# Optimization experiments

Hardware: AMD Instinct MI355X
Metric: run time of the kernel (lower is better)

Reference implementation:

```python
import jax, jax.numpy as jnp
import numpy as np

NEG = -9e15

def setup_inputs() -> dict:
    key = jax.random.key(0)
    kH, kA, kW, ka = jax.random.split(key, 4)
    B, N, Din, Dout, Hh = 4, 2048, 128, 32, 8
    H = jax.random.normal(kH, (B, N, Din), dtype=jnp.float32)
    adj = jax.random.randint(kA, (B, N, N), 0, 2, dtype=jnp.int32)
    W = jax.random.normal(kW, (Hh, Din, Dout), dtype=jnp.float32) * (1.0 / np.sqrt(Din))
    a = jax.random.normal(ka, (Hh, 2 * Dout, 1), dtype=jnp.float32) * 0.1
    return {"H": H, "adj": adj, "W": W, "a": a}

def reference(H, adj, W, a):
    # H: [B,N,Din], adj: [B,N,N], W: [h,Din,D], a: [h,2D,1]
    B, N, _ = H.shape
    h, _, D = W.shape
    Wh = jnp.einsum('bni,hio->bhno', H, W)            # [B,h,N,D]
    a1 = a[:, :D, 0]                                   # [h,D] (source/query half)
    a2 = a[:, D:, 0]                                   # [h,D] (neighbor half)
    ei = jnp.einsum('bhnd,hd->bhn', Wh, a1)            # [B,h,N]
    ej = jnp.einsum('bhnd,hd->bhn', Wh, a2)            # [B,h,N]
    e = ei[:, :, :, None] + ej[:, :, None, :]          # [B,h,N,N] == a^T[Wh_i;Wh_j]
    mask = adj[:, None, :, :].astype(bool)             # [B,1,N,N]
    e = jnp.where(mask, e, jnp.float32(NEG))
    alpha = jax.nn.softmax(e, axis=-1)                 # [B,h,N,N]; dropout is identity (eval)
    h_prime = jnp.einsum('bhnm,bhmd->bhnd', alpha, Wh) # [B,h,N,D]
    h_prime = jnp.transpose(h_prime, (0, 2, 1, 3)).reshape(B, N, h * D)
    return jax.nn.relu(h_prime), alpha
```

## Files before the change

kernel.cpp:

```cpp
#include <hip/hip_runtime.h>
#include <stdint.h>

#define BB 4
#define NN 2048
#define DIN 128
#define DOUT 32
#define HH 8
#define NW 64

typedef __bf16 bf16x8 __attribute__((ext_vector_type(8)));
typedef float  f32x4  __attribute__((ext_vector_type(4)));

static __device__ __forceinline__ unsigned short f2b(float f) {
    __bf16 h = (__bf16)f;
    return __builtin_bit_cast(unsigned short, h);
}
static __device__ __forceinline__ float b2f(unsigned short u) {
    union { unsigned int i; float f; } v; v.i = ((unsigned int)u) << 16; return v.f;
}

__global__ __launch_bounds__(256) void k_wht(const float* __restrict__ Hg,
                                             const float* __restrict__ Wg,
                                             unsigned short* __restrict__ WhT)
{
    __shared__ float Hs[DIN * 16];
    const int t  = threadIdx.x;
    const int b  = blockIdx.x >> 7;
    const int n0 = (blockIdx.x & 127) << 4;

    {
        const int r = t >> 4, i0 = (t & 15) << 3;
        const float4* hp = (const float4*)(Hg + ((size_t)(b * NN + n0 + r)) * DIN + i0);
        float4 u0 = hp[0], u1 = hp[1];
        float vv[8] = { u0.x, u0.y, u0.z, u0.w, u1.x, u1.y, u1.z, u1.w };
#pragma unroll
        for (int j = 0; j < 8; j++) Hs[(i0 + j) * 16 + r] = vv[j];
    }
    __syncthreads();

    const int h = t >> 5, d = t & 31;
    f32x4 a0 = {0,0,0,0}, a1 = {0,0,0,0}, a2 = {0,0,0,0}, a3 = {0,0,0,0};
    const float* wp = Wg + h * DIN * DOUT + d;
#pragma unroll 8
    for (int i = 0; i < DIN; i++) {
        float wv = wp[i * DOUT];
        const f32x4* hr = (const f32x4*)&Hs[i * 16];
        a0 += wv * hr[0];
        a1 += wv * hr[1];
        a2 += wv * hr[2];
        a3 += wv * hr[3];
    }
    float v[16] = { a0[0],a0[1],a0[2],a0[3], a1[0],a1[1],a1[2],a1[3],
                    a2[0],a2[1],a2[2],a2[3], a3[0],a3[1],a3[2],a3[3] };
    unsigned int pw[8];
#pragma unroll
    for (int j = 0; j < 8; j++)
        pw[j] = (unsigned int)f2b(v[2*j]) | ((unsigned int)f2b(v[2*j+1]) << 16);
    uint4* dst = (uint4*)(WhT + ((size_t)((b * HH + h) * DOUT + d)) * NN + n0);
    dst[0] = make_uint4(pw[0], pw[1], pw[2], pw[3]);
    dst[1] = make_uint4(pw[4], pw[5], pw[6], pw[7]);
}

__global__ __launch_bounds__(256) void k_bits(const int* __restrict__ adj,
                                              unsigned long long* __restrict__ BM)
{
    size_t tg = (size_t)blockIdx.x * 256 + threadIdx.x;
    unsigned long long m = __ballot(adj[tg] != 0);
    if ((threadIdx.x & 63) == 0) BM[tg >> 6] = m;
}

__global__ __launch_bounds__(256) void k_e(const unsigned short* __restrict__ WhT,
                                           const float* __restrict__ ag,
                                           float* __restrict__ E)
{
    const int blk = blockIdx.x;
    const int bh  = blk >> 3;
    const int h   = bh & 7;
    const int m   = ((blk & 7) << 8) + threadIdx.x;
    const unsigned short* wp = WhT + (size_t)(bh * DOUT) * NN + m;
    float acc = 0.f;
#pragma unroll 8
    for (int dd = 0; dd < DOUT; dd++)
        acc += b2f(wp[(size_t)dd * NN]) * ag[h * 2 * DOUT + DOUT + dd];
    E[(size_t)bh * NN + m] = __expf(acc);
}

__global__ __launch_bounds__(256) void k_main(const float* __restrict__ E,
                                              const unsigned int* __restrict__ BM,
                                              const unsigned short* __restrict__ WhT,
                                              float* __restrict__ out0,
                                              float* __restrict__ out1)
{
    __shared__ float        Es[NN];
    __shared__ unsigned int bits[16][68];
    __shared__ float        red[16][17];
    __shared__ float        invS[16];
    __shared__ __align__(16) __bf16 Ast[4][16][72];
    __shared__ __align__(16) __bf16 Bst[4][32][72];
    __shared__ float        Cred[4][16][33];

    const int t   = threadIdx.x;
    const int bh  = blockIdx.x >> 7;
    const int b   = bh >> 3, h = bh & 7;
    const int n0  = (blockIdx.x & 127) << 4;

    {
        const f32x4* src = (const f32x4*)(E + (size_t)bh * NN);
        f32x4* dst = (f32x4*)Es;
        dst[t]       = src[t];
        dst[t + 256] = src[t + 256];
        const int r = t >> 4, w0 = (t & 15) << 2;
        *(uint4*)&bits[r][w0] =
            *(const uint4*)(BM + ((size_t)(b * NN + n0 + r)) * NW + w0);
    }
    __syncthreads();

    {
        const int r = t >> 4, l = t & 15;
        const unsigned int* br = bits[r];
        float s = 0.f;
#pragma unroll 4
        for (int k2 = 0; k2 < NW; k2++) {
            unsigned int wd = br[k2];
            int m = (k2 << 5) + l;
            if ((wd >> l) & 1)        s += Es[m];
            if ((wd >> (l + 16)) & 1) s += Es[m + 16];
        }
        red[r][l] = s;
    }
    __syncthreads();
    if (t < 16) {
        float s = 0.f;
#pragma unroll
        for (int j = 0; j < 16; j++) s += red[t][j];
        invS[t] = 1.0f / s;
    }
    __syncthreads();

    const int w = t >> 6, lane = t & 63;
    const int r2 = lane >> 2, c4 = lane & 3;
    const int quad = lane >> 4, l16 = lane & 15;
    f32x4 acc[2] = { {0,0,0,0}, {0,0,0,0} };
    const size_t out1row = ((size_t)bh * NN + n0 + r2) * NN;
    const unsigned short* wsrc = WhT + ((size_t)bh * DOUT + (lane >> 1)) * NN
                                     + ((lane & 1) << 5);

    for (int c = 0; c < 8; c++) {
        const int m0 = (w << 9) + (c << 6);
        const int mL = m0 + (c4 << 4);

        {
            const float iv = invS[r2];
            const unsigned int wv =
                (bits[r2][(m0 >> 5) + (c4 >> 1)] >> ((c4 & 1) << 4)) & 0xFFFFu;
            const f32x4* ev = (const f32x4*)&Es[mL];
            float* orow = out1 + out1row + mL;
            unsigned int pk[8];
#pragma unroll
            for (int q = 0; q < 4; q++) {
                f32x4 e4 = ev[q];
                f32x4 x;
                x[0] = ((wv >> (4*q + 0)) & 1) ? e4[0] * iv : 0.f;
                x[1] = ((wv >> (4*q + 1)) & 1) ? e4[1] * iv : 0.f;
                x[2] = ((wv >> (4*q + 2)) & 1) ? e4[2] * iv : 0.f;
                x[3] = ((wv >> (4*q + 3)) & 1) ? e4[3] * iv : 0.f;
                *(f32x4*)(orow + (q << 2)) = x;
                pk[2*q]     = (unsigned int)f2b(x[0]) | ((unsigned int)f2b(x[1]) << 16);
                pk[2*q + 1] = (unsigned int)f2b(x[2]) | ((unsigned int)f2b(x[3]) << 16);
            }
            uint4 q0 = make_uint4(pk[0], pk[1], pk[2], pk[3]);
            uint4 q1 = make_uint4(pk[4], pk[5], pk[6], pk[7]);
            *(bf16x8*)&Ast[w][r2][(c4 << 4)]     = __builtin_bit_cast(bf16x8, q0);
            *(bf16x8*)&Ast[w][r2][(c4 << 4) + 8] = __builtin_bit_cast(bf16x8, q1);
        }

        {
            const uint4* s4 = (const uint4*)(wsrc + m0);
            __bf16* dp = &Bst[w][lane >> 1][(lane & 1) << 5];
#pragma unroll
            for (int k = 0; k < 4; k++)
                *(bf16x8*)(dp + 8*k) = __builtin_bit_cast(bf16x8, s4[k]);
        }

#pragma unroll
        for (int ks = 0; ks < 64; ks += 32) {
            bf16x8 af  = *(const bf16x8*)&Ast[w][l16     ][ks + (quad << 3)];
            bf16x8 bf0 = *(const bf16x8*)&Bst[w][l16     ][ks + (quad << 3)];
            bf16x8 bf1 = *(const bf16x8*)&Bst[w][l16 + 16][ks + (quad << 3)];
            acc[0] = __builtin_amdgcn_mfma_f32_16x16x32_bf16(af, bf0, acc[0], 0, 0, 0);
            acc[1] = __builtin_amdgcn_mfma_f32_16x16x32_bf16(af, bf1, acc[1], 0, 0, 0);
        }
    }

#pragma unroll
    for (int hf = 0; hf < 2; hf++)
#pragma unroll
        for (int i = 0; i < 4; i++)
            Cred[w][(quad << 2) + i][l16 + (hf << 4)] = acc[hf][i];
    __syncthreads();
#pragma unroll
    for (int e = t; e < 512; e += 256) {
        const int r = e >> 5, d = e & 31;
        float v = Cred[0][r][d] + Cred[1][r][d] + Cred[2][r][d] + Cred[3][r][d];
        out0[((size_t)(b * NN + n0 + r)) * (HH * DOUT) + h * DOUT + d] = fmaxf(v, 0.f);
    }
}

extern "C" void kernel_launch(void* const* d_in, const int* in_sizes, int n_in,
                              void* d_out, int out_size, void* d_ws, size_t ws_size,
                              hipStream_t stream)
{
    const float* Hg  = (const float*)d_in[0];
    const int*   adj = (const int*)d_in[1];
    const float* Wg  = (const float*)d_in[2];
    const float* ag  = (const float*)d_in[3];

    float* out0 = (float*)d_out;
    float* out1 = out0 + (size_t)BB * NN * HH * DOUT;

    char* ws = (char*)d_ws;
    unsigned short* WhT = (unsigned short*)ws;
    float*          E   = (float*)(ws + (size_t)BB*HH*DOUT*NN*2);
    unsigned int*   BM  = (unsigned int*)(ws + (size_t)BB*HH*DOUT*NN*2
                                             + (size_t)BB*HH*NN*4);

    k_wht <<<BB * (NN/16),         256, 0, stream>>>(Hg, Wg, WhT);
    k_bits<<<(BB * NN * NN) / 256, 256, 0, stream>>>(adj, (unsigned long long*)BM);
    k_e   <<<BB * HH * (NN/256),   256, 0, stream>>>(WhT, ag, E);
    k_main<<<BB * HH * (NN/16),    256, 0, stream>>>(E, BM, WhT, out0, out1);
}
```

Measured before the change: 709.0 us.

## Fuse exp-score kernel into projection and feed MFMA straight from registers

Computes the neighbor attention term and its exponential inside the projection kernel, which removes the separate E kernel and its re-read of WhT. The main kernel now builds MFMA A and B operands directly in registers, using a lane mapping that matches the MFMA input layout, so the shared-memory staging buffers are gone. Alpha rows are written with nontemporal stores. The cost is extra shared memory and a barrier in the projection kernel, plus uncoalesced-looking direct global loads of WhT for the B operand.

```diff
diff --git a/kernel.cpp b/kernel.cpp
--- a/kernel.cpp
+++ b/kernel.cpp
@@ -15,15 +15,15 @@
     __bf16 h = (__bf16)f;
     return __builtin_bit_cast(unsigned short, h);
 }
-static __device__ __forceinline__ float b2f(unsigned short u) {
-    union { unsigned int i; float f; } v; v.i = ((unsigned int)u) << 16; return v.f;
-}
 
 __global__ __launch_bounds__(256) void k_wht(const float* __restrict__ Hg,
                                              const float* __restrict__ Wg,
-                                             unsigned short* __restrict__ WhT)
+                                             const float* __restrict__ ag,
+                                             unsigned short* __restrict__ WhT,
+                                             float* __restrict__ E)
 {
     __shared__ float Hs[DIN * 16];
+    __shared__ float ejred[HH][16][36];
     const int t  = threadIdx.x;
     const int b  = blockIdx.x >> 7;
     const int n0 = (blockIdx.x & 127) << 4;
@@ -59,6 +59,18 @@
     uint4* dst = (uint4*)(WhT + ((size_t)((b * HH + h) * DOUT + d)) * NN + n0);
     dst[0] = make_uint4(pw[0], pw[1], pw[2], pw[3]);
     dst[1] = make_uint4(pw[4], pw[5], pw[6], pw[7]);
+
+    const float a2v = ag[h * 2 * DOUT + DOUT + d];
+#pragma unroll
+    for (int j = 0; j < 16; j++) ejred[h][j][d] = v[j] * a2v;
+    __syncthreads();
+    if (t < 128) {
+        const int hh = t >> 4, j = t & 15;
+        const f32x4* rp = (const f32x4*)&ejred[hh][j][0];
+        f32x4 s4 = rp[0] + rp[1] + rp[2] + rp[3] + rp[4] + rp[5] + rp[6] + rp[7];
+        float s = s4[0] + s4[1] + s4[2] + s4[3];
+        E[((size_t)(b * HH + hh)) * NN + n0 + j] = __expf(s);
+    }
 }
 
 __global__ __launch_bounds__(256) void k_bits(const int* __restrict__ adj,
@@ -67,22 +79,6 @@
     size_t tg = (size_t)blockIdx.x * 256 + threadIdx.x;
     unsigned long long m = __ballot(adj[tg] != 0);
     if ((threadIdx.x & 63) == 0) BM[tg >> 6] = m;
-}
-
-__global__ __launch_bounds__(256) void k_e(const unsigned short* __restrict__ WhT,
-                                           const float* __restrict__ ag,
-                                           float* __restrict__ E)
-{
-    const int blk = blockIdx.x;
-    const int bh  = blk >> 3;
-    const int h   = bh & 7;
-    const int m   = ((blk & 7) << 8) + threadIdx.x;
-    const unsigned short* wp = WhT + (size_t)(bh * DOUT) * NN + m;
-    float acc = 0.f;
-#pragma unroll 8
-    for (int dd = 0; dd < DOUT; dd++)
-        acc += b2f(wp[(size_t)dd * NN]) * ag[h * 2 * DOUT + DOUT + dd];
-    E[(size_t)bh * NN + m] = __expf(acc);
 }
 
 __global__ __launch_bounds__(256) void k_main(const float* __restrict__ E,
@@ -95,8 +91,6 @@
     __shared__ unsigned int bits[16][68];
     __shared__ float        red[16][17];
     __shared__ float        invS[16];
-    __shared__ __align__(16) __bf16 Ast[4][16][72];
-    __shared__ __align__(16) __bf16 Bst[4][32][72];
     __shared__ float        Cred[4][16][33];
 
     const int t   = threadIdx.x;
@@ -138,58 +132,59 @@
     __syncthreads();
 
     const int w = t >> 6, lane = t & 63;
-    const int r2 = lane >> 2, c4 = lane & 3;
     const int quad = lane >> 4, l16 = lane & 15;
     f32x4 acc[2] = { {0,0,0,0}, {0,0,0,0} };
-    const size_t out1row = ((size_t)bh * NN + n0 + r2) * NN;
-    const unsigned short* wsrc = WhT + ((size_t)bh * DOUT + (lane >> 1)) * NN
-                                     + ((lane & 1) << 5);
-
+    const float iv = invS[l16];
+    float* o1 = out1 + ((size_t)bh * NN + n0 + l16) * NN;
+    const unsigned short* wB0 = WhT + ((size_t)(bh * DOUT) + l16) * NN;
+    const unsigned short* wB1 = wB0 + (size_t)16 * NN;
+
+#pragma unroll 2
     for (int c = 0; c < 8; c++) {
         const int m0 = (w << 9) + (c << 6);
-        const int mL = m0 + (c4 << 4);
-
-        {
-            const float iv = invS[r2];
-            const unsigned int wv =
-                (bits[r2][(m0 >> 5) + (c4 >> 1)] >> ((c4 & 1) << 4)) & 0xFFFFu;
-            const f32x4* ev = (const f32x4*)&Es[mL];
-            float* orow = out1 + out1row + mL;
-            unsigned int pk[8];
-#pragma unroll
-            for (int q = 0; q < 4; q++) {
-                f32x4 e4 = ev[q];
-                f32x4 x;
-                x[0] = ((wv >> (4*q + 0)) & 1) ? e4[0] * iv : 0.f;
-                x[1] = ((wv >> (4*q + 1)) & 1) ? e4[1] * iv : 0.f;
-                x[2] = ((wv >> (4*q + 2)) & 1) ? e4[2] * iv : 0.f;
-                x[3] = ((wv >> (4*q + 3)) & 1) ? e4[3] * iv : 0.f;
-                *(f32x4*)(orow + (q << 2)) = x;
-                pk[2*q]     = (unsigned int)f2b(x[0]) | ((unsigned int)f2b(x[1]) << 16);
-                pk[2*q + 1] = (unsigned int)f2b(x[2]) | ((unsigned int)f2b(x[3]) << 16);
-            }
-            uint4 q0 = make_uint4(pk[0], pk[1], pk[2], pk[3]);
-            uint4 q1 = make_uint4(pk[4], pk[5], pk[6], pk[7]);
-            *(bf16x8*)&Ast[w][r2][(c4 << 4)]     = __builtin_bit_cast(bf16x8, q0);
-            *(bf16x8*)&Ast[w][r2][(c4 << 4) + 8] = __builtin_bit_cast(bf16x8, q1);
+        const uint2 bw = *(const uint2*)&bits[l16][m0 >> 5];
+        const unsigned int b0 = bw.x >> (quad << 3);
+        const unsigned int b1 = bw.y >> (quad << 3);
+
+        const int mA = m0 + (quad << 3);
+        f32x4 e0 = *(const f32x4*)&Es[mA];
+        f32x4 e1 = *(const f32x4*)&Es[mA + 4];
+        f32x4 e2 = *(const f32x4*)&Es[mA + 32];
+        f32x4 e3 = *(const f32x4*)&Es[mA + 36];
+        f32x4 x0, x1, x2, x3;
+#pragma unroll
+        for (int j = 0; j < 4; j++) {
+            x0[j] = ((b0 >> j) & 1)       ? e0[j] * iv : 0.f;
+            x1[j] = ((b0 >> (j + 4)) & 1) ? e1[j] * iv : 0.f;
+            x2[j] = ((b1 >> j) & 1)       ? e2[j] * iv : 0.f;
+            x3[j] = ((b1 >> (j + 4)) & 1) ? e3[j] * iv : 0.f;
         }
-
-        {
-            const uint4* s4 = (const uint4*)(wsrc + m0);
-            __bf16* dp = &Bst[w][lane >> 1][(lane & 1) << 5];
-#pragma unroll
-            for (int k = 0; k < 4; k++)
-                *(bf16x8*)(dp + 8*k) = __builtin_bit_cast(bf16x8, s4[k]);
-        }
-
-#pragma unroll
-        for (int ks = 0; ks < 64; ks += 32) {
-            bf16x8 af  = *(const bf16x8*)&Ast[w][l16     ][ks + (quad << 3)];
-            bf16x8 bf0 = *(const bf16x8*)&Bst[w][l16     ][ks + (quad << 3)];
-            bf16x8 bf1 = *(const bf16x8*)&Bst[w][l16 + 16][ks + (quad << 3)];
-            acc[0] = __builtin_amdgcn_mfma_f32_16x16x32_bf16(af, bf0, acc[0], 0, 0, 0);
-            acc[1] = __builtin_amdgcn_mfma_f32_16x16x32_bf16(af, bf1, acc[1], 0, 0, 0);
-        }
+        __builtin_nontemporal_store(x0, (f32x4*)(o1 + mA));
+        __builtin_nontemporal_store(x1, (f32x4*)(o1 + mA + 4));
+        __builtin_nontemporal_store(x2, (f32x4*)(o1 + mA + 32));
+        __builtin_nontemporal_store(x3, (f32x4*)(o1 + mA + 36));
+
+        unsigned int pk[8] = {
+            (unsigned int)f2b(x0[0]) | ((unsigned int)f2b(x0[1]) << 16),
+            (unsigned int)f2b(x0[2]) | ((unsigned int)f2b(x0[3]) << 16),
+            (unsigned int)f2b(x1[0]) | ((unsigned int)f2b(x1[1]) << 16),
+            (unsigned int)f2b(x1[2]) | ((unsigned int)f2b(x1[3]) << 16),
+            (unsigned int)f2b(x2[0]) | ((unsigned int)f2b(x2[1]) << 16),
+            (unsigned int)f2b(x2[2]) | ((unsigned int)f2b(x2[3]) << 16),
+            (unsigned int)f2b(x3[0]) | ((unsigned int)f2b(x3[1]) << 16),
+            (unsigned int)f2b(x3[2]) | ((unsigned int)f2b(x3[3]) << 16) };
+        bf16x8 af0 = __builtin_bit_cast(bf16x8, make_uint4(pk[0], pk[1], pk[2], pk[3]));
+        bf16x8 af1 = __builtin_bit_cast(bf16x8, make_uint4(pk[4], pk[5], pk[6], pk[7]));
+
+        bf16x8 b00 = __builtin_bit_cast(bf16x8, *(const uint4*)(wB0 + mA));
+        bf16x8 b01 = __builtin_bit_cast(bf16x8, *(const uint4*)(wB0 + mA + 32));
+        bf16x8 b10 = __builtin_bit_cast(bf16x8, *(const uint4*)(wB1 + mA));
+        bf16x8 b11 = __builtin_bit_cast(bf16x8, *(const uint4*)(wB1 + mA + 32));
+
+        acc[0] = __builtin_amdgcn_mfma_f32_16x16x32_bf16(af0, b00, acc[0], 0, 0, 0);
+        acc[1] = __builtin_amdgcn_mfma_f32_16x16x32_bf16(af0, b10, acc[1], 0, 0, 0);
+        acc[0] = __builtin_amdgcn_mfma_f32_16x16x32_bf16(af1, b01, acc[0], 0, 0, 0);
+        acc[1] = __builtin_amdgcn_mfma_f32_16x16x32_bf16(af1, b11, acc[1], 0, 0, 0);
     }
 
 #pragma unroll
@@ -224,8 +219,7 @@
     unsigned int*   BM  = (unsigned int*)(ws + (size_t)BB*HH*DOUT*NN*2
                                              + (size_t)BB*HH*NN*4);
 
-    k_wht <<<BB * (NN/16),         256, 0, stream>>>(Hg, Wg, WhT);
+    k_wht <<<BB * (NN/16),         256, 0, stream>>>(Hg, Wg, ag, WhT, E);
     k_bits<<<(BB * NN * NN) / 256, 256, 0, stream>>>(adj, (unsigned long long*)BM);
-    k_e   <<<BB * HH * (NN/256),   256, 0, stream>>>(WhT, ag, E);
     k_main<<<BB * HH * (NN/16),    256, 0, stream>>>(E, BM, WhT, out0, out1);
 }
```

Result: no change. 722.9 us (+2.0%).
